# Performance work log

Measured on AMD Instinct MI355X. Metric: run time of the kernel, lower is better.

The kernel has to match this reference:

```python
import jax, jax.numpy as jnp
import numpy as np

B, L, D_MODEL, D_FF, N_EXPERTS, TOP_K = 32, 256, 512, 2048, 8, 2
EPS = 1e-9


def setup_inputs() -> dict:
    key = jax.random.key(0)
    ks = jax.random.split(key, 7)
    scale1 = 1.0 / np.sqrt(D_MODEL)
    scale2 = 1.0 / np.sqrt(D_FF)
    return {
        "cycle_curve_data": jax.random.normal(ks[0], (B, L, D_MODEL), jnp.float32),
        "logits": jax.random.normal(ks[1], (B, N_EXPERTS), jnp.float32),
        "moe_masks": jax.random.randint(ks[2], (B, N_EXPERTS), 0, 2, jnp.int32),
        "W1": jax.random.normal(ks[3], (N_EXPERTS, D_MODEL, D_FF), jnp.float32) * scale1,
        "b1": jax.random.normal(ks[4], (N_EXPERTS, D_FF), jnp.float32) * scale1,
        "W2": jax.random.normal(ks[5], (N_EXPERTS, D_FF, D_MODEL), jnp.float32) * scale2,
        "b2": jax.random.normal(ks[6], (N_EXPERTS, D_MODEL), jnp.float32) * scale2,
    }


def _gates(logits, moe_masks):
    # softmax over experts, zero out unavailable experts, keep top-k, renormalize
    mask = (moe_masks == 1).astype(logits.dtype)               # [B, E]
    p = jax.nn.softmax(logits, axis=1) * mask                  # [B, E]
    _, idx = jax.lax.top_k(p, TOP_K)                           # [B, K]
    topk_mask = jnp.zeros_like(p).at[jnp.arange(p.shape[0])[:, None], idx].set(1.0)
    p = p * topk_mask
    return p / (jnp.sum(p, axis=1, keepdims=True) + EPS)       # [B, E]


def reference(cycle_curve_data, logits, moe_masks, W1, b1, W2, b2):
    gates = _gates(logits, moe_masks)                          # [B, E]
    x = cycle_curve_data                                       # [B, L, D]
    # dense equivalent of per-expert gather -> MLP -> gate-weighted scatter-combine
    h = jnp.einsum("bld,edf->eblf", x, W1) + b1[:, None, None, :]   # [E,B,L,F]
    h = jax.nn.gelu(h, approximate=False)
    out = jnp.einsum("be,eblf,efd->bld", gates, h, W2)
    out = out + jnp.einsum("be,ed->bd", gates, b2)[:, None, :]      # [B,L,D]
    return out
```

## Files before the change

kernel.cpp:

```cpp
#include <hip/hip_runtime.h>

#define B_SZ 32
#define L_SZ 256
#define D_SZ 512
#define F_SZ 2048
#define E_SZ 8
#define P_SZ 64
#define BK   32

typedef __attribute__((ext_vector_type(8))) short bf16x8;
typedef __attribute__((ext_vector_type(4))) float f32x4;

__device__ __forceinline__ unsigned short f2bf(float f) {
  unsigned int u = __builtin_bit_cast(unsigned int, f);
  u += 0x7fffu + ((u >> 16) & 1u);
  return (unsigned short)(u >> 16);
}

__device__ __forceinline__ void async16(const void* g, void* l) {
  __builtin_amdgcn_global_load_lds(
      (const __attribute__((address_space(1))) unsigned int*)g,
      (__attribute__((address_space(3))) unsigned int*)l, 16, 0, 0);
}

__global__ void gates_kernel(const float* __restrict__ logits,
                             const int* __restrict__ masks,
                             int* __restrict__ sel_e,
                             float* __restrict__ sel_g) {
  int b = threadIdx.x;
  if (b >= B_SZ) return;
  float lg[E_SZ], p[E_SZ];
  float mx = -1e30f;
  for (int e = 0; e < E_SZ; ++e) { lg[e] = logits[b * E_SZ + e]; mx = fmaxf(mx, lg[e]); }
  float s = 0.f;
  for (int e = 0; e < E_SZ; ++e) { p[e] = expf(lg[e] - mx); s += p[e]; }
  for (int e = 0; e < E_SZ; ++e) p[e] = (masks[b * E_SZ + e] == 1) ? (p[e] / s) : 0.f;
  int i0 = 0, i1 = 1; float v0 = -1.f, v1 = -1.f;
  for (int e = 0; e < E_SZ; ++e) {
    float v = p[e];
    if (v > v0)      { v1 = v0; i1 = i0; v0 = v; i0 = e; }
    else if (v > v1) { v1 = v;  i1 = e; }
  }
  float den = v0 + v1 + 1e-9f;
  sel_e[2 * b]     = i0;  sel_e[2 * b + 1] = i1;
  sel_g[2 * b]     = v0 / den;
  sel_g[2 * b + 1] = v1 / den;
}

__global__ void convert_f32_bf16(const float* __restrict__ in,
                                 unsigned short* __restrict__ out, int n4) {
  int i = blockIdx.x * blockDim.x + threadIdx.x;
  if (i >= n4) return;
  float4 v = ((const float4*)in)[i];
  ushort4 o;
  o.x = f2bf(v.x); o.y = f2bf(v.y); o.z = f2bf(v.z); o.w = f2bf(v.w);
  ((ushort4*)out)[i] = o;
}

__global__ void transpose_convert(const float* __restrict__ in,
                                  unsigned short* __restrict__ out,
                                  int R, int C) {
  __shared__ float tile[64][65];
  const float* ip = in + (size_t)blockIdx.z * R * C;
  unsigned short* op = out + (size_t)blockIdx.z * R * C;
  int c0 = blockIdx.x * 64, r0 = blockIdx.y * 64;
  int tx = threadIdx.x & 63, ty = threadIdx.x >> 6;
#pragma unroll
  for (int i = 0; i < 16; ++i) {
    int r = i * 4 + ty;
    tile[r][tx] = ip[(size_t)(r0 + r) * C + c0 + tx];
  }
  __syncthreads();
#pragma unroll
  for (int i = 0; i < 16; ++i) {
    int rr = i * 4 + ty;
    op[(size_t)(c0 + rr) * R + r0 + tx] = f2bf(tile[tx][rr]);
  }
}

__global__ __launch_bounds__(256, 2) void moe_gemm1(
    const unsigned short* __restrict__ Xb,
    const unsigned short* __restrict__ W1t,
    const float* __restrict__ b1,
    const int* __restrict__ sel_e,
    unsigned short* __restrict__ H) {
  int p = blockIdx.z;
  int b = p >> 1;
  int e = sel_e[p];
  int f0 = blockIdx.x * 128;
  int l0 = blockIdx.y * 128;

  __shared__ __align__(16) unsigned short As[128 * BK];
  __shared__ __align__(16) unsigned short Bs[128 * BK];

  const unsigned short* Abase = Xb  + ((size_t)b * L_SZ + l0) * D_SZ;
  const unsigned short* Bbase = W1t + ((size_t)e * F_SZ + f0) * D_SZ;

  int tid = threadIdx.x;
  int lane = tid & 63;
  int w = tid >> 6, wm = w & 1, wn = w >> 1;
  int lrow = lane & 15, kg = lane >> 4;

  int seg0 = w * 128 + lane;
  int row0 = seg0 >> 2, ks0 = (seg0 & 3) * 8;
  int seg1 = seg0 + 64;
  int row1 = seg1 >> 2, ks1 = (seg1 & 3) * 8;

  f32x4 acc[4][4] = {};

  for (int k0 = 0; k0 < D_SZ; k0 += BK) {
    async16(Abase + (size_t)row0 * D_SZ + k0 + ks0, &As[seg0 * 8]);
    async16(Abase + (size_t)row1 * D_SZ + k0 + ks1, &As[seg1 * 8]);
    async16(Bbase + (size_t)row0 * D_SZ + k0 + ks0, &Bs[seg0 * 8]);
    async16(Bbase + (size_t)row1 * D_SZ + k0 + ks1, &Bs[seg1 * 8]);
    __syncthreads();
    bf16x8 af[4], bfr[4];
#pragma unroll
    for (int i = 0; i < 4; ++i)
      af[i] = *(const bf16x8*)&As[(wm * 64 + i * 16 + lrow) * BK + kg * 8];
#pragma unroll
    for (int j = 0; j < 4; ++j)
      bfr[j] = *(const bf16x8*)&Bs[(wn * 64 + j * 16 + lrow) * BK + kg * 8];
#pragma unroll
    for (int i = 0; i < 4; ++i)
#pragma unroll
      for (int j = 0; j < 4; ++j)
        acc[i][j] = __builtin_amdgcn_mfma_f32_16x16x32_bf16(af[i], bfr[j], acc[i][j], 0, 0, 0);
    __syncthreads();
  }

  unsigned short* Hp = H + ((size_t)p * L_SZ + l0) * F_SZ + f0;
  float b1v[4];
#pragma unroll
  for (int j = 0; j < 4; ++j)
    b1v[j] = b1[e * F_SZ + f0 + wn * 64 + j * 16 + lrow];
#pragma unroll
  for (int i = 0; i < 4; ++i) {
    int rbase = wm * 64 + i * 16 + kg * 4;
#pragma unroll
    for (int j = 0; j < 4; ++j) {
      int c = wn * 64 + j * 16 + lrow;
#pragma unroll
      for (int r = 0; r < 4; ++r) {
        float v = acc[i][j][r] + b1v[j];
        v = 0.5f * v * (1.0f + erff(v * 0.70710678118654752f));
        Hp[(size_t)(rbase + r) * F_SZ + c] = f2bf(v);
      }
    }
  }
}

__global__ __launch_bounds__(256, 2) void moe_gemm2(
    const unsigned short* __restrict__ H,
    const unsigned short* __restrict__ W2t,
    const float* __restrict__ b2,
    const int* __restrict__ sel_e,
    const float* __restrict__ sel_g,
    float* __restrict__ Out) {
  int b = blockIdx.z;
  int d0 = blockIdx.x * 128;
  int l0 = blockIdx.y * 128;

  __shared__ __align__(16) unsigned short As[128 * BK];
  __shared__ __align__(16) unsigned short Bs[128 * BK];

  int tid = threadIdx.x;
  int lane = tid & 63;
  int w = tid >> 6, wm = w & 1, wn = w >> 1;
  int lrow = lane & 15, kg = lane >> 4;
  int seg0 = w * 128 + lane;
  int row0 = seg0 >> 2, ks0 = (seg0 & 3) * 8;
  int seg1 = seg0 + 64;
  int row1 = seg1 >> 2, ks1 = (seg1 & 3) * 8;

  float cv[4][4][4] = {};

  for (int jp = 0; jp < 2; ++jp) {
    int p = 2 * b + jp;
    int e = sel_e[p];
    float g = sel_g[p];
    const unsigned short* Abase = H   + ((size_t)p * L_SZ + l0) * F_SZ;
    const unsigned short* Bbase = W2t + ((size_t)e * D_SZ + d0) * F_SZ;
    f32x4 acc[4][4] = {};
    for (int k0 = 0; k0 < F_SZ; k0 += BK) {
      async16(Abase + (size_t)row0 * F_SZ + k0 + ks0, &As[seg0 * 8]);
      async16(Abase + (size_t)row1 * F_SZ + k0 + ks1, &As[seg1 * 8]);
      async16(Bbase + (size_t)row0 * F_SZ + k0 + ks0, &Bs[seg0 * 8]);
      async16(Bbase + (size_t)row1 * F_SZ + k0 + ks1, &Bs[seg1 * 8]);
      __syncthreads();
      bf16x8 af[4], bfr[4];
#pragma unroll
      for (int i = 0; i < 4; ++i)
        af[i] = *(const bf16x8*)&As[(wm * 64 + i * 16 + lrow) * BK + kg * 8];
#pragma unroll
      for (int j = 0; j < 4; ++j)
        bfr[j] = *(const bf16x8*)&Bs[(wn * 64 + j * 16 + lrow) * BK + kg * 8];
#pragma unroll
      for (int i = 0; i < 4; ++i)
#pragma unroll
        for (int j = 0; j < 4; ++j)
          acc[i][j] = __builtin_amdgcn_mfma_f32_16x16x32_bf16(af[i], bfr[j], acc[i][j], 0, 0, 0);
      __syncthreads();
    }
#pragma unroll
    for (int i = 0; i < 4; ++i)
#pragma unroll
      for (int j = 0; j < 4; ++j)
#pragma unroll
        for (int r = 0; r < 4; ++r)
          cv[i][j][r] += g * acc[i][j][r];
  }

  int e0 = sel_e[2 * b], e1 = sel_e[2 * b + 1];
  float g0 = sel_g[2 * b], g1 = sel_g[2 * b + 1];
  float bias[4];
#pragma unroll
  for (int j = 0; j < 4; ++j) {
    int d = d0 + wn * 64 + j * 16 + lrow;
    bias[j] = g0 * b2[e0 * D_SZ + d] + g1 * b2[e1 * D_SZ + d];
  }
  float* Op = Out + ((size_t)b * L_SZ + l0) * D_SZ + d0;
#pragma unroll
  for (int i = 0; i < 4; ++i) {
    int rbase = wm * 64 + i * 16 + kg * 4;
#pragma unroll
    for (int j = 0; j < 4; ++j) {
      int c = wn * 64 + j * 16 + lrow;
#pragma unroll
      for (int r = 0; r < 4; ++r)
        Op[(size_t)(rbase + r) * D_SZ + c] = cv[i][j][r] + bias[j];
    }
  }
}

extern "C" void kernel_launch(void* const* d_in, const int* in_sizes, int n_in,
                              void* d_out, int out_size, void* d_ws, size_t ws_size,
                              hipStream_t stream) {
  const float* x      = (const float*)d_in[0];
  const float* logits = (const float*)d_in[1];
  const int*   masks  = (const int*)d_in[2];
  const float* W1     = (const float*)d_in[3];
  const float* b1     = (const float*)d_in[4];
  const float* W2     = (const float*)d_in[5];
  const float* b2     = (const float*)d_in[6];
  float* out = (float*)d_out;

  char* ws = (char*)d_ws;
  int*   sel_e = (int*)ws;
  float* sel_g = (float*)(ws + 256);
  unsigned short* xb  = (unsigned short*)(ws + 1024);
  unsigned short* w1t = xb  + (size_t)B_SZ * L_SZ * D_SZ;
  unsigned short* w2t = w1t + (size_t)E_SZ * F_SZ * D_SZ;
  unsigned short* Hbuf = w2t + (size_t)E_SZ * D_SZ * F_SZ;

  gates_kernel<<<1, 64, 0, stream>>>(logits, masks, sel_e, sel_g);

  int n4 = (B_SZ * L_SZ * D_SZ) / 4;
  convert_f32_bf16<<<n4 / 256, 256, 0, stream>>>(x, xb, n4);

  transpose_convert<<<dim3(F_SZ / 64, D_SZ / 64, E_SZ), 256, 0, stream>>>(W1, w1t, D_SZ, F_SZ);
  transpose_convert<<<dim3(D_SZ / 64, F_SZ / 64, E_SZ), 256, 0, stream>>>(W2, w2t, F_SZ, D_SZ);

  moe_gemm1<<<dim3(F_SZ / 128, L_SZ / 128, P_SZ), 256, 0, stream>>>(xb, w1t, b1, sel_e, Hbuf);
  moe_gemm2<<<dim3(D_SZ / 128, L_SZ / 128, B_SZ), 256, 0, stream>>>(Hbuf, w2t, b2, sel_e, sel_g, out);
}
```

Measured before the change: 278.5 us.

## Split-K gemm2 with atomic accumulation, fast GELU, vectorized transpose, higher occupancy

gemm2 now launches one block per (pair, K-half) rather than per batch. Each block atomically adds its gate-scaled partial into an output that a new bias_init kernel fills beforehand with the gated b2 bias. This gives four times as many blocks and better GPU fill, at the cost of float atomics and a nondeterministic summation order. The erff GELU is replaced with a polynomial approximation (Abramowitz–Stegun) using fast rcp and exp. The weight transpose becomes a per-thread gather of 8 rows with one vector store, and launch bounds are raised to 4 blocks per CU.

```diff
diff --git a/kernel.cpp b/kernel.cpp
--- a/kernel.cpp
+++ b/kernel.cpp
@@ -10,6 +10,7 @@
 
 typedef __attribute__((ext_vector_type(8))) short bf16x8;
 typedef __attribute__((ext_vector_type(4))) float f32x4;
+typedef __attribute__((ext_vector_type(8))) unsigned short u16x8;
 
 __device__ __forceinline__ unsigned short f2bf(float f) {
   unsigned int u = __builtin_bit_cast(unsigned int, f);
@@ -21,6 +22,20 @@
   __builtin_amdgcn_global_load_lds(
       (const __attribute__((address_space(1))) unsigned int*)g,
       (__attribute__((address_space(3))) unsigned int*)l, 16, 0, 0);
+}
+
+__device__ __forceinline__ float gelu_f(float x) {
+  float a = fabsf(x) * 0.70710678118654752f;
+  float t = __builtin_amdgcn_rcpf(1.0f + 0.3275911f * a);
+  float y = t * (0.254829592f +
+            t * (-0.284496736f +
+            t * (1.421413741f +
+            t * (-1.453152027f +
+            t * 1.061405429f))));
+  float e = __expf(-a * a);
+  float erf_abs = 1.0f - y * e;
+  float erf_v = (x < 0.f) ? -erf_abs : erf_abs;
+  return 0.5f * x * (1.0f + erf_v);
 }
 
 __global__ void gates_kernel(const float* __restrict__ logits,
@@ -60,25 +75,37 @@
 __global__ void transpose_convert(const float* __restrict__ in,
                                   unsigned short* __restrict__ out,
                                   int R, int C) {
-  __shared__ float tile[64][65];
-  const float* ip = in + (size_t)blockIdx.z * R * C;
-  unsigned short* op = out + (size_t)blockIdx.z * R * C;
-  int c0 = blockIdx.x * 64, r0 = blockIdx.y * 64;
-  int tx = threadIdx.x & 63, ty = threadIdx.x >> 6;
-#pragma unroll
-  for (int i = 0; i < 16; ++i) {
-    int r = i * 4 + ty;
-    tile[r][tx] = ip[(size_t)(r0 + r) * C + c0 + tx];
-  }
-  __syncthreads();
-#pragma unroll
-  for (int i = 0; i < 16; ++i) {
-    int rr = i * 4 + ty;
-    op[(size_t)(c0 + rr) * R + r0 + tx] = f2bf(tile[tx][rr]);
-  }
-}
-
-__global__ __launch_bounds__(256, 2) void moe_gemm1(
+  int t = blockIdx.x * blockDim.x + threadIdx.x;
+  int c  = t & (C - 1);
+  int r8 = (t / C) & (R / 8 - 1);
+  int z  = t / (C * (R / 8));
+  const float* ip = in + (size_t)z * R * C + (size_t)(r8 * 8) * C + c;
+  u16x8 o;
+#pragma unroll
+  for (int i = 0; i < 8; ++i) o[i] = f2bf(ip[(size_t)i * C]);
+  *(u16x8*)(out + (size_t)z * C * R + (size_t)c * R + r8 * 8) = o;
+}
+
+__global__ void bias_init(const float* __restrict__ b2,
+                          const int* __restrict__ sel_e,
+                          const float* __restrict__ sel_g,
+                          float* __restrict__ out) {
+  int i = blockIdx.x * blockDim.x + threadIdx.x;
+  int d4 = i & (D_SZ / 4 - 1);
+  int b  = i >> (7 + 8);
+  int e0 = sel_e[2 * b], e1 = sel_e[2 * b + 1];
+  float g0 = sel_g[2 * b], g1 = sel_g[2 * b + 1];
+  float4 v0 = ((const float4*)(b2 + (size_t)e0 * D_SZ))[d4];
+  float4 v1 = ((const float4*)(b2 + (size_t)e1 * D_SZ))[d4];
+  float4 r;
+  r.x = g0 * v0.x + g1 * v1.x;
+  r.y = g0 * v0.y + g1 * v1.y;
+  r.z = g0 * v0.z + g1 * v1.z;
+  r.w = g0 * v0.w + g1 * v1.w;
+  ((float4*)out)[i] = r;
+}
+
+__global__ __launch_bounds__(256, 4) void moe_gemm1(
     const unsigned short* __restrict__ Xb,
     const unsigned short* __restrict__ W1t,
     const float* __restrict__ b1,
@@ -142,22 +169,24 @@
       int c = wn * 64 + j * 16 + lrow;
 #pragma unroll
       for (int r = 0; r < 4; ++r) {
-        float v = acc[i][j][r] + b1v[j];
-        v = 0.5f * v * (1.0f + erff(v * 0.70710678118654752f));
+        float v = gelu_f(acc[i][j][r] + b1v[j]);
         Hp[(size_t)(rbase + r) * F_SZ + c] = f2bf(v);
       }
     }
   }
 }
 
-__global__ __launch_bounds__(256, 2) void moe_gemm2(
+__global__ __launch_bounds__(256, 4) void moe_gemm2(
     const unsigned short* __restrict__ H,
     const unsigned short* __restrict__ W2t,
-    const float* __restrict__ b2,
     const int* __restrict__ sel_e,
     const float* __restrict__ sel_g,
     float* __restrict__ Out) {
-  int b = blockIdx.z;
+  int zz = blockIdx.z;
+  int p = zz >> 1, kh = zz & 1;
+  int b = p >> 1;
+  int e = sel_e[p];
+  float g = sel_g[p];
   int d0 = blockIdx.x * 128;
   int l0 = blockIdx.y * 128;
 
@@ -173,52 +202,31 @@
   int seg1 = seg0 + 64;
   int row1 = seg1 >> 2, ks1 = (seg1 & 3) * 8;
 
-  float cv[4][4][4] = {};
-
-  for (int jp = 0; jp < 2; ++jp) {
-    int p = 2 * b + jp;
-    int e = sel_e[p];
-    float g = sel_g[p];
-    const unsigned short* Abase = H   + ((size_t)p * L_SZ + l0) * F_SZ;
-    const unsigned short* Bbase = W2t + ((size_t)e * D_SZ + d0) * F_SZ;
-    f32x4 acc[4][4] = {};
-    for (int k0 = 0; k0 < F_SZ; k0 += BK) {
-      async16(Abase + (size_t)row0 * F_SZ + k0 + ks0, &As[seg0 * 8]);
-      async16(Abase + (size_t)row1 * F_SZ + k0 + ks1, &As[seg1 * 8]);
-      async16(Bbase + (size_t)row0 * F_SZ + k0 + ks0, &Bs[seg0 * 8]);
-      async16(Bbase + (size_t)row1 * F_SZ + k0 + ks1, &Bs[seg1 * 8]);
-      __syncthreads();
-      bf16x8 af[4], bfr[4];
-#pragma unroll
-      for (int i = 0; i < 4; ++i)
-        af[i] = *(const bf16x8*)&As[(wm * 64 + i * 16 + lrow) * BK + kg * 8];
+  const unsigned short* Abase = H   + ((size_t)p * L_SZ + l0) * F_SZ + kh * (F_SZ / 2);
+  const unsigned short* Bbase = W2t + ((size_t)e * D_SZ + d0) * F_SZ + kh * (F_SZ / 2);
+
+  f32x4 acc[4][4] = {};
+  for (int k0 = 0; k0 < F_SZ / 2; k0 += BK) {
+    async16(Abase + (size_t)row0 * F_SZ + k0 + ks0, &As[seg0 * 8]);
+    async16(Abase + (size_t)row1 * F_SZ + k0 + ks1, &As[seg1 * 8]);
+    async16(Bbase + (size_t)row0 * F_SZ + k0 + ks0, &Bs[seg0 * 8]);
+    async16(Bbase + (size_t)row1 * F_SZ + k0 + ks1, &Bs[seg1 * 8]);
+    __syncthreads();
+    bf16x8 af[4], bfr[4];
+#pragma unroll
+    for (int i = 0; i < 4; ++i)
+      af[i] = *(const bf16x8*)&As[(wm * 64 + i * 16 + lrow) * BK + kg * 8];
+#pragma unroll
+    for (int j = 0; j < 4; ++j)
+      bfr[j] = *(const bf16x8*)&Bs[(wn * 64 + j * 16 + lrow) * BK + kg * 8];
+#pragma unroll
+    for (int i = 0; i < 4; ++i)
 #pragma unroll
       for (int j = 0; j < 4; ++j)
-        bfr[j] = *(const bf16x8*)&Bs[(wn * 64 + j * 16 + lrow) * BK + kg * 8];
-#pragma unroll
-      for (int i = 0; i < 4; ++i)
-#pragma unroll
-        for (int j = 0; j < 4; ++j)
-          acc[i][j] = __builtin_amdgcn_mfma_f32_16x16x32_bf16(af[i], bfr[j], acc[i][j], 0, 0, 0);
-      __syncthreads();
-    }
-#pragma unroll
-    for (int i = 0; i < 4; ++i)
-#pragma unroll
-      for (int j = 0; j < 4; ++j)
-#pragma unroll
-        for (int r = 0; r < 4; ++r)
-          cv[i][j][r] += g * acc[i][j][r];
-  }
-
-  int e0 = sel_e[2 * b], e1 = sel_e[2 * b + 1];
-  float g0 = sel_g[2 * b], g1 = sel_g[2 * b + 1];
-  float bias[4];
-#pragma unroll
-  for (int j = 0; j < 4; ++j) {
-    int d = d0 + wn * 64 + j * 16 + lrow;
-    bias[j] = g0 * b2[e0 * D_SZ + d] + g1 * b2[e1 * D_SZ + d];
-  }
+        acc[i][j] = __builtin_amdgcn_mfma_f32_16x16x32_bf16(af[i], bfr[j], acc[i][j], 0, 0, 0);
+    __syncthreads();
+  }
+
   float* Op = Out + ((size_t)b * L_SZ + l0) * D_SZ + d0;
 #pragma unroll
   for (int i = 0; i < 4; ++i) {
@@ -228,7 +236,7 @@
       int c = wn * 64 + j * 16 + lrow;
 #pragma unroll
       for (int r = 0; r < 4; ++r)
-        Op[(size_t)(rbase + r) * D_SZ + c] = cv[i][j][r] + bias[j];
+        unsafeAtomicAdd(&Op[(size_t)(rbase + r) * D_SZ + c], g * acc[i][j][r]);
     }
   }
 }
@@ -258,9 +266,11 @@
   int n4 = (B_SZ * L_SZ * D_SZ) / 4;
   convert_f32_bf16<<<n4 / 256, 256, 0, stream>>>(x, xb, n4);
 
-  transpose_convert<<<dim3(F_SZ / 64, D_SZ / 64, E_SZ), 256, 0, stream>>>(W1, w1t, D_SZ, F_SZ);
-  transpose_convert<<<dim3(D_SZ / 64, F_SZ / 64, E_SZ), 256, 0, stream>>>(W2, w2t, F_SZ, D_SZ);
+  transpose_convert<<<(E_SZ * F_SZ * (D_SZ / 8)) / 256, 256, 0, stream>>>(W1, w1t, D_SZ, F_SZ);
+  transpose_convert<<<(E_SZ * D_SZ * (F_SZ / 8)) / 256, 256, 0, stream>>>(W2, w2t, F_SZ, D_SZ);
+
+  bias_init<<<(B_SZ * L_SZ * D_SZ / 4) / 256, 256, 0, stream>>>(b2, sel_e, sel_g, out);
 
   moe_gemm1<<<dim3(F_SZ / 128, L_SZ / 128, P_SZ), 256, 0, stream>>>(xb, w1t, b1, sel_e, Hbuf);
-  moe_gemm2<<<dim3(D_SZ / 128, L_SZ / 128, B_SZ), 256, 0, stream>>>(Hbuf, w2t, b2, sel_e, sel_g, out);
-}
+  moe_gemm2<<<dim3(D_SZ / 128, L_SZ / 128, P_SZ * 2), 256, 0, stream>>>(Hbuf, w2t, sel_e, sel_g, out);
+}
```

New measurement: 302.0 us. 1.08x slower.
